# Optimization experiments

Hardware: AMD Instinct MI355X
Metric: run time of the kernel (lower is better)

Reference implementation:

```python
import jax, jax.numpy as jnp
import numpy as np

B, T = 16, 2048
NEG = -1e9  # finite large-negative for masked softmax (avoids NaN on empty rows)


def setup_inputs() -> dict:
    key = jax.random.key(0)
    k1, k2 = jax.random.split(key)
    logits = jax.random.normal(k1, (B, T, 1), dtype=jnp.float32)
    seq_len = jax.random.randint(k2, (B,), 1, T + 1, dtype=jnp.int32)
    return {"logits": logits, "seq_len": seq_len}


def reference(logits, seq_len):
    scores = jax.nn.sigmoid(logits.squeeze(-1))  # [B, T]
    # pairwise relevance: sigmoid((1 - |s_i - s_j| - 0.5) / 0.1)
    pairwise_diff = scores[:, :, None] - scores[:, None, :]  # [B, T, T]
    rel_mat = jax.nn.sigmoid((1.0 - jnp.abs(pairwise_diff) - 0.5) / 0.1)
    # ragged mask: valid positions are < seq_len[b]
    valid = jnp.arange(T)[None, :] < seq_len[:, None]            # [B, T]
    mask2d = valid[:, :, None] & valid[:, None, :]               # [B, T, T]
    masked = jnp.where(mask2d, rel_mat, NEG)
    sm = jax.nn.softmax(masked, axis=-1)                          # masked cols -> ~0
    # zero out invalid rows (original leaves them as zeros)
    out_mat = jnp.where(valid[:, :, None], sm, 0.0)
    return out_mat
```

## Files before the change

### kernel.cpp

```cpp
#include <hip/hip_runtime.h>

#define TT 2048
#define BLOCK 256
#define WAVES (BLOCK / 64)

#define LOG2E 1.4426950408889634f

typedef float vf4 __attribute__((ext_vector_type(4)));

__device__ __forceinline__ void nt_store4(float4* p, float x, float y, float z, float w) {
    vf4 v = {x, y, z, w};
    __builtin_nontemporal_store(v, (vf4*)p);
}

__device__ __forceinline__ float fast_sigmoid_e2(float u) {
    return __builtin_amdgcn_rcpf(1.0f + __builtin_amdgcn_exp2f(u));
}

__global__ __launch_bounds__(BLOCK) void score_branch_kernel(
    const float* __restrict__ logits, const int* __restrict__ seq_len,
    float* __restrict__ out)
{
    __shared__ float s_scores[TT];

    const int b    = blockIdx.y;
    const int row0 = blockIdx.x * WAVES;
    const int tid  = threadIdx.x;
    const int lane = tid & 63;
    const int wv   = tid >> 6;
    const int L    = seq_len[b];

    const int i = row0 + wv;
    float4* orow4 = (float4*)(out + ((size_t)b * TT + (size_t)i) * TT);

    if (row0 >= L) {
        #pragma unroll
        for (int q = 0; q < 8; ++q)
            nt_store4(&orow4[q * 64 + lane], 0.f, 0.f, 0.f, 0.f);
        return;
    }

    const float4* lg4 = (const float4*)(logits + (size_t)b * TT);
    float4* s4 = (float4*)s_scores;
    #pragma unroll
    for (int k = 0; k < TT / (BLOCK * 4); ++k) {
        int idx4 = tid + k * BLOCK;
        if (idx4 * 4 < L) {
            float4 v = lg4[idx4];
            float4 s;
            s.x = fast_sigmoid_e2(-LOG2E * v.x);
            s.y = fast_sigmoid_e2(-LOG2E * v.y);
            s.z = fast_sigmoid_e2(-LOG2E * v.z);
            s.w = fast_sigmoid_e2(-LOG2E * v.w);
            s4[idx4] = s;
        }
    }
    __syncthreads();

    if (i >= L) {
        #pragma unroll
        for (int q = 0; q < 8; ++q)
            nt_store4(&orow4[q * 64 + lane], 0.f, 0.f, 0.f, 0.f);
        return;
    }

    #pragma unroll
    for (int q = 0; q < 8; ++q) {
        if (q * 256 >= L)
            nt_store4(&orow4[q * 64 + lane], 0.f, 0.f, 0.f, 0.f);
    }

    const float si = s_scores[i];

    float4 e4[8];
    float partial = 0.f;
    #pragma unroll
    for (int q = 0; q < 8; ++q) {
        if (q * 256 < L) {
            const int idx4 = q * 64 + lane;
            float4 sj = s4[idx4];
            const int j0 = idx4 * 4;
            const bool fullgrp = ((q + 1) * 256 <= L);
            float vals[4] = {sj.x, sj.y, sj.z, sj.w};
            float* ev = (float*)&e4[q];
            #pragma unroll
            for (int qq = 0; qq < 4; ++qq) {
                float d  = si - vals[qq];
                float u  = fmaf(fabsf(d), 10.0f * LOG2E, -5.0f * LOG2E);
                float p  = fast_sigmoid_e2(u);
                float ee = __builtin_amdgcn_exp2f(p * LOG2E);
                if (!fullgrp)
                    ee = (j0 + qq < L) ? ee : 0.0f;
                ev[qq] = ee;
                partial += ee;
            }
        }
    }

    #pragma unroll
    for (int off = 32; off > 0; off >>= 1)
        partial += __shfl_xor(partial, off, 64);
    const float inv = __builtin_amdgcn_rcpf(partial);

    #pragma unroll
    for (int q = 0; q < 8; ++q) {
        if (q * 256 < L) {
            nt_store4(&orow4[q * 64 + lane],
                      e4[q].x * inv, e4[q].y * inv, e4[q].z * inv, e4[q].w * inv);
        }
    }
}

extern "C" void kernel_launch(void* const* d_in, const int* in_sizes, int n_in,
                              void* d_out, int out_size, void* d_ws, size_t ws_size,
                              hipStream_t stream) {
    const float* logits  = (const float*)d_in[0];
    const int*   seq_len = (const int*)d_in[1];
    float*       out     = (float*)d_out;

    const int B = in_sizes[1];
    dim3 grid(TT / WAVES, B);
    score_branch_kernel<<<grid, dim3(BLOCK), 0, stream>>>(logits, seq_len, out);
}
```

Before: 265.7 us.

## Split into prep (row sums) and emit kernels; use regular stores

Splits the fused softmax kernel into two launches. A prep kernel computes the sigmoid scores and each row's reciprocal softmax sum into workspace, and an emit kernel recomputes the exponentials and writes the normalized output directly, so no per-row register array is kept. Nontemporal stores are also replaced with plain float4 stores. The split doubles the transcendental work and adds a launch, in exchange for lower register pressure and a simpler store stream.

```diff
diff --git a/kernel.cpp b/kernel.cpp
--- a/kernel.cpp
+++ b/kernel.cpp
@@ -2,26 +2,20 @@
 
 #define TT 2048
 #define BLOCK 256
-#define WAVES (BLOCK / 64)
+#define WAVES 4
 
 #define LOG2E 1.4426950408889634f
 
-typedef float vf4 __attribute__((ext_vector_type(4)));
-
-__device__ __forceinline__ void nt_store4(float4* p, float x, float y, float z, float w) {
-    vf4 v = {x, y, z, w};
-    __builtin_nontemporal_store(v, (vf4*)p);
-}
-
-__device__ __forceinline__ float fast_sigmoid_e2(float u) {
+__device__ __forceinline__ float sig_e2(float u) {
     return __builtin_amdgcn_rcpf(1.0f + __builtin_amdgcn_exp2f(u));
 }
 
-__global__ __launch_bounds__(BLOCK) void score_branch_kernel(
+__global__ __launch_bounds__(BLOCK) void prep_kernel(
     const float* __restrict__ logits, const int* __restrict__ seq_len,
-    float* __restrict__ out)
+    float* __restrict__ ws_scores,
+    float* __restrict__ ws_inv)
 {
-    __shared__ float s_scores[TT];
+    __shared__ float s_sc[TT];
 
     const int b    = blockIdx.y;
     const int row0 = blockIdx.x * WAVES;
@@ -30,48 +24,169 @@
     const int wv   = tid >> 6;
     const int L    = seq_len[b];
 
+    const float4* lg4 = (const float4*)(logits + (size_t)b * TT);
+    float4* s4 = (float4*)s_sc;
+    #pragma unroll
+    for (int k = 0; k < 2; ++k) {
+        int idx4 = tid + k * BLOCK;
+        float4 v = lg4[idx4];
+        float4 s;
+        s.x = sig_e2(-LOG2E * v.x);
+        s.y = sig_e2(-LOG2E * v.y);
+        s.z = sig_e2(-LOG2E * v.z);
+        s.w = sig_e2(-LOG2E * v.w);
+        s4[idx4] = s;
+        if (blockIdx.x == 0)
+            ((float4*)(ws_scores + (size_t)b * TT))[idx4] = s;
+    }
+    __syncthreads();
+
+    const int i = row0 + wv;
+    if (i >= L) return;
+
+    const float si = s_sc[i];
+    float partial = 0.f;
+    #pragma unroll
+    for (int q = 0; q < 8; ++q) {
+        if (q * 256 < L) {
+            const int idx4 = q * 64 + lane;
+            float4 sj = s4[idx4];
+            const int j0 = idx4 * 4;
+            const bool fullgrp = ((q + 1) * 256 <= L);
+            float vals[4] = {sj.x, sj.y, sj.z, sj.w};
+            #pragma unroll
+            for (int qq = 0; qq < 4; ++qq) {
+                float d  = si - vals[qq];
+                float u  = fmaf(fabsf(d), 10.0f * LOG2E, -5.0f * LOG2E);
+                float p  = sig_e2(u);
+                float ee = __builtin_amdgcn_exp2f(p * LOG2E);
+                if (!fullgrp)
+                    ee = (j0 + qq < L) ? ee : 0.0f;
+                partial += ee;
+            }
+        }
+    }
+    #pragma unroll
+    for (int off = 32; off > 0; off >>= 1)
+        partial += __shfl_xor(partial, off, 64);
+    if (lane == 0)
+        ws_inv[(size_t)b * TT + i] = __builtin_amdgcn_rcpf(partial);
+}
+
+__global__ __launch_bounds__(BLOCK) void emit_kernel(
+    const int* __restrict__ seq_len,
+    const float* __restrict__ ws_scores, const float* __restrict__ ws_inv,
+    float* __restrict__ out)
+{
+    __shared__ float s_sc[TT];
+
+    const int b    = blockIdx.y;
+    const int row0 = blockIdx.x * WAVES;
+    const int tid  = threadIdx.x;
+    const int lane = tid & 63;
+    const int wv   = tid >> 6;
+    const int L    = seq_len[b];
+
     const int i = row0 + wv;
     float4* orow4 = (float4*)(out + ((size_t)b * TT + (size_t)i) * TT);
+    const float4 z4 = make_float4(0.f, 0.f, 0.f, 0.f);
 
     if (row0 >= L) {
         #pragma unroll
         for (int q = 0; q < 8; ++q)
-            nt_store4(&orow4[q * 64 + lane], 0.f, 0.f, 0.f, 0.f);
-        return;
-    }
-
+            orow4[q * 64 + lane] = z4;
+        return;
+    }
+
+    const float4* sc4 = (const float4*)(ws_scores + (size_t)b * TT);
+    float4* s4 = (float4*)s_sc;
+    #pragma unroll
+    for (int k = 0; k < 2; ++k) {
+        int idx4 = tid + k * BLOCK;
+        s4[idx4] = sc4[idx4];
+    }
+    __syncthreads();
+
+    if (i >= L) {
+        #pragma unroll
+        for (int q = 0; q < 8; ++q)
+            orow4[q * 64 + lane] = z4;
+        return;
+    }
+
+    #pragma unroll
+    for (int q = 0; q < 8; ++q)
+        if (q * 256 >= L)
+            orow4[q * 64 + lane] = z4;
+
+    const float si  = s_sc[i];
+    const float inv = ws_inv[(size_t)b * TT + i];
+
+    #pragma unroll
+    for (int q = 0; q < 8; ++q) {
+        if (q * 256 < L) {
+            const int idx4 = q * 64 + lane;
+            float4 sj = s4[idx4];
+            const int j0 = idx4 * 4;
+            const bool fullgrp = ((q + 1) * 256 <= L);
+            float vals[4] = {sj.x, sj.y, sj.z, sj.w};
+            float4 o;
+            float* ov = (float*)&o;
+            #pragma unroll
+            for (int qq = 0; qq < 4; ++qq) {
+                float d  = si - vals[qq];
+                float u  = fmaf(fabsf(d), 10.0f * LOG2E, -5.0f * LOG2E);
+                float p  = sig_e2(u);
+                float ee = __builtin_amdgcn_exp2f(p * LOG2E);
+                if (!fullgrp)
+                    ee = (j0 + qq < L) ? ee : 0.0f;
+                ov[qq] = ee * inv;
+            }
+            orow4[idx4] = o;
+        }
+    }
+}
+
+__global__ __launch_bounds__(BLOCK) void score_branch_kernel(
+    const float* __restrict__ logits, const int* __restrict__ seq_len,
+    float* __restrict__ out)
+{
+    __shared__ float s_scores[TT];
+    const int b    = blockIdx.y;
+    const int row0 = blockIdx.x * WAVES;
+    const int tid  = threadIdx.x;
+    const int lane = tid & 63;
+    const int wv   = tid >> 6;
+    const int L    = seq_len[b];
+    const int i = row0 + wv;
+    float4* orow4 = (float4*)(out + ((size_t)b * TT + (size_t)i) * TT);
+    const float4 z4 = make_float4(0.f, 0.f, 0.f, 0.f);
+
+    if (row0 >= L) {
+        #pragma unroll
+        for (int q = 0; q < 8; ++q) orow4[q * 64 + lane] = z4;
+        return;
+    }
     const float4* lg4 = (const float4*)(logits + (size_t)b * TT);
     float4* s4 = (float4*)s_scores;
     #pragma unroll
-    for (int k = 0; k < TT / (BLOCK * 4); ++k) {
+    for (int k = 0; k < 2; ++k) {
         int idx4 = tid + k * BLOCK;
-        if (idx4 * 4 < L) {
-            float4 v = lg4[idx4];
-            float4 s;
-            s.x = fast_sigmoid_e2(-LOG2E * v.x);
-            s.y = fast_sigmoid_e2(-LOG2E * v.y);
-            s.z = fast_sigmoid_e2(-LOG2E * v.z);
-            s.w = fast_sigmoid_e2(-LOG2E * v.w);
-            s4[idx4] = s;
-        }
+        float4 v = lg4[idx4];
+        float4 s;
+        s.x = sig_e2(-LOG2E * v.x);
+        s.y = sig_e2(-LOG2E * v.y);
+        s.z = sig_e2(-LOG2E * v.z);
+        s.w = sig_e2(-LOG2E * v.w);
+        s4[idx4] = s;
     }
     __syncthreads();
-
     if (i >= L) {
         #pragma unroll
-        for (int q = 0; q < 8; ++q)
-            nt_store4(&orow4[q * 64 + lane], 0.f, 0.f, 0.f, 0.f);
-        return;
-    }
-
-    #pragma unroll
-    for (int q = 0; q < 8; ++q) {
-        if (q * 256 >= L)
-            nt_store4(&orow4[q * 64 + lane], 0.f, 0.f, 0.f, 0.f);
-    }
-
+        for (int q = 0; q < 8; ++q) orow4[q * 64 + lane] = z4;
+        return;
+    }
     const float si = s_scores[i];
-
     float4 e4[8];
     float partial = 0.f;
     #pragma unroll
@@ -87,26 +202,27 @@
             for (int qq = 0; qq < 4; ++qq) {
                 float d  = si - vals[qq];
                 float u  = fmaf(fabsf(d), 10.0f * LOG2E, -5.0f * LOG2E);
-                float p  = fast_sigmoid_e2(u);
+                float p  = sig_e2(u);
                 float ee = __builtin_amdgcn_exp2f(p * LOG2E);
-                if (!fullgrp)
-                    ee = (j0 + qq < L) ? ee : 0.0f;
+                if (!fullgrp) ee = (j0 + qq < L) ? ee : 0.0f;
                 ev[qq] = ee;
                 partial += ee;
             }
-        }
-    }
-
+        } else {
+            orow4[q * 64 + lane] = z4;
+        }
+    }
     #pragma unroll
     for (int off = 32; off > 0; off >>= 1)
         partial += __shfl_xor(partial, off, 64);
     const float inv = __builtin_amdgcn_rcpf(partial);
-
-    #pragma unroll
-    for (int q = 0; q < 8; ++q) {
-        if (q * 256 < L) {
-            nt_store4(&orow4[q * 64 + lane],
-                      e4[q].x * inv, e4[q].y * inv, e4[q].z * inv, e4[q].w * inv);
+    #pragma unroll
+    for (int q = 0; q < 8; ++q) {
+        if (q * 256 < L) {
+            float4 o;
+            o.x = e4[q].x * inv; o.y = e4[q].y * inv;
+            o.z = e4[q].z * inv; o.w = e4[q].w * inv;
+            orow4[q * 64 + lane] = o;
         }
     }
 }
@@ -119,6 +235,15 @@
     float*       out     = (float*)d_out;
 
     const int B = in_sizes[1];
-    dim3 grid(TT / WAVES, B);
-    score_branch_kernel<<<grid, dim3(BLOCK), 0, stream>>>(logits, seq_len, out);
-}
+    dim3 grid(TT / WAVES, B), blk(BLOCK);
+
+    const size_t need = (size_t)2 * B * TT * sizeof(float);
+    if (d_ws != nullptr && ws_size >= need) {
+        float* ws_scores = (float*)d_ws;
+        float* ws_inv    = ws_scores + (size_t)B * TT;
+        prep_kernel<<<grid, blk, 0, stream>>>(logits, seq_len, ws_scores, ws_inv);
+        emit_kernel<<<grid, blk, 0, stream>>>(seq_len, ws_scores, ws_inv, out);
+    } else {
+        score_branch_kernel<<<grid, blk, 0, stream>>>(logits, seq_len, out);
+    }
+}
```

Measured after the change: 272.9 us. 1.03x slower.

## Process eight rows per wave to amortize score staging; use regular stores

Applied to the files above, without the earlier changes.

Each wave now handles eight consecutive rows, so a block covers 32 rows and the grid shrinks eightfold. Each block's sigmoid staging of the scores into shared memory is therefore reused across more rows. The staging loop also drops its length guard and sigmoids all 2048 logits. Nontemporal stores are replaced with ordinary float4 stores, which changes cache behaviour on a write-bound 256MB output and may cost something. Fewer blocks also means less parallelism and worse load balance across ragged rows.

```diff
diff --git a/kernel.cpp b/kernel.cpp
--- a/kernel.cpp
+++ b/kernel.cpp
@@ -2,18 +2,13 @@
 
 #define TT 2048
 #define BLOCK 256
-#define WAVES (BLOCK / 64)
+#define WAVES 4
+#define RPW 8
+#define ROWS_PER_BLOCK (WAVES * RPW)
 
 #define LOG2E 1.4426950408889634f
 
-typedef float vf4 __attribute__((ext_vector_type(4)));
-
-__device__ __forceinline__ void nt_store4(float4* p, float x, float y, float z, float w) {
-    vf4 v = {x, y, z, w};
-    __builtin_nontemporal_store(v, (vf4*)p);
-}
-
-__device__ __forceinline__ float fast_sigmoid_e2(float u) {
+__device__ __forceinline__ float sig_e2(float u) {
     return __builtin_amdgcn_rcpf(1.0f + __builtin_amdgcn_exp2f(u));
 }
 
@@ -21,92 +16,97 @@
     const float* __restrict__ logits, const int* __restrict__ seq_len,
     float* __restrict__ out)
 {
-    __shared__ float s_scores[TT];
+    __shared__ float s_sc[TT];
 
     const int b    = blockIdx.y;
-    const int row0 = blockIdx.x * WAVES;
+    const int row0 = blockIdx.x * ROWS_PER_BLOCK;
     const int tid  = threadIdx.x;
     const int lane = tid & 63;
     const int wv   = tid >> 6;
     const int L    = seq_len[b];
 
-    const int i = row0 + wv;
-    float4* orow4 = (float4*)(out + ((size_t)b * TT + (size_t)i) * TT);
+    const int wrow0 = row0 + wv * RPW;
+    const float4 z4 = make_float4(0.f, 0.f, 0.f, 0.f);
 
     if (row0 >= L) {
-        #pragma unroll
-        for (int q = 0; q < 8; ++q)
-            nt_store4(&orow4[q * 64 + lane], 0.f, 0.f, 0.f, 0.f);
+        float4* o4 = (float4*)(out + ((size_t)b * TT + wrow0) * TT);
+        for (int r = 0; r < RPW; ++r) {
+            #pragma unroll
+            for (int q = 0; q < 8; ++q)
+                o4[r * (TT / 4) + q * 64 + lane] = z4;
+        }
         return;
     }
 
     const float4* lg4 = (const float4*)(logits + (size_t)b * TT);
-    float4* s4 = (float4*)s_scores;
+    float4* s4 = (float4*)s_sc;
     #pragma unroll
-    for (int k = 0; k < TT / (BLOCK * 4); ++k) {
+    for (int k = 0; k < 2; ++k) {
         int idx4 = tid + k * BLOCK;
-        if (idx4 * 4 < L) {
-            float4 v = lg4[idx4];
-            float4 s;
-            s.x = fast_sigmoid_e2(-LOG2E * v.x);
-            s.y = fast_sigmoid_e2(-LOG2E * v.y);
-            s.z = fast_sigmoid_e2(-LOG2E * v.z);
-            s.w = fast_sigmoid_e2(-LOG2E * v.w);
-            s4[idx4] = s;
-        }
+        float4 v = lg4[idx4];
+        float4 s;
+        s.x = sig_e2(-LOG2E * v.x);
+        s.y = sig_e2(-LOG2E * v.y);
+        s.z = sig_e2(-LOG2E * v.z);
+        s.w = sig_e2(-LOG2E * v.w);
+        s4[idx4] = s;
     }
     __syncthreads();
 
-    if (i >= L) {
+    for (int r = 0; r < RPW; ++r) {
+        const int i = wrow0 + r;
+        float4* orow4 = (float4*)(out + ((size_t)b * TT + (size_t)i) * TT);
+
+        if (i >= L) {
+            #pragma unroll
+            for (int q = 0; q < 8; ++q)
+                orow4[q * 64 + lane] = z4;
+            continue;
+        }
+
+        const float si = s_sc[i];
+        float4 e4[8];
+        float partial = 0.f;
         #pragma unroll
-        for (int q = 0; q < 8; ++q)
-            nt_store4(&orow4[q * 64 + lane], 0.f, 0.f, 0.f, 0.f);
-        return;
-    }
-
-    #pragma unroll
-    for (int q = 0; q < 8; ++q) {
-        if (q * 256 >= L)
-            nt_store4(&orow4[q * 64 + lane], 0.f, 0.f, 0.f, 0.f);
-    }
-
-    const float si = s_scores[i];
-
-    float4 e4[8];
-    float partial = 0.f;
-    #pragma unroll
-    for (int q = 0; q < 8; ++q) {
-        if (q * 256 < L) {
-            const int idx4 = q * 64 + lane;
-            float4 sj = s4[idx4];
-            const int j0 = idx4 * 4;
-            const bool fullgrp = ((q + 1) * 256 <= L);
-            float vals[4] = {sj.x, sj.y, sj.z, sj.w};
-            float* ev = (float*)&e4[q];
-            #pragma unroll
-            for (int qq = 0; qq < 4; ++qq) {
-                float d  = si - vals[qq];
-                float u  = fmaf(fabsf(d), 10.0f * LOG2E, -5.0f * LOG2E);
-                float p  = fast_sigmoid_e2(u);
-                float ee = __builtin_amdgcn_exp2f(p * LOG2E);
-                if (!fullgrp)
-                    ee = (j0 + qq < L) ? ee : 0.0f;
-                ev[qq] = ee;
-                partial += ee;
+        for (int q = 0; q < 8; ++q) {
+            if (q * 256 < L) {
+                const int idx4 = q * 64 + lane;
+                float4 sj = s4[idx4];
+                const int j0 = idx4 * 4;
+                const bool fullgrp = ((q + 1) * 256 <= L);
+                float vals[4] = {sj.x, sj.y, sj.z, sj.w};
+                float* ev = (float*)&e4[q];
+                #pragma unroll
+                for (int qq = 0; qq < 4; ++qq) {
+                    float d  = si - vals[qq];
+                    float u  = fmaf(fabsf(d), 10.0f * LOG2E, -5.0f * LOG2E);
+                    float p  = sig_e2(u);
+                    float ee = __builtin_amdgcn_exp2f(p * LOG2E);
+                    if (!fullgrp)
+                        ee = (j0 + qq < L) ? ee : 0.0f;
+                    ev[qq] = ee;
+                    partial += ee;
+                }
+            } else {
+                orow4[q * 64 + lane] = z4;
             }
         }
-    }
 
-    #pragma unroll
-    for (int off = 32; off > 0; off >>= 1)
-        partial += __shfl_xor(partial, off, 64);
-    const float inv = __builtin_amdgcn_rcpf(partial);
+        #pragma unroll
+        for (int off = 32; off > 0; off >>= 1)
+            partial += __shfl_xor(partial, off, 64);
+        const float inv = __builtin_amdgcn_rcpf(partial);
 
-    #pragma unroll
-    for (int q = 0; q < 8; ++q) {
-        if (q * 256 < L) {
-            nt_store4(&orow4[q * 64 + lane],
-                      e4[q].x * inv, e4[q].y * inv, e4[q].z * inv, e4[q].w * inv);
+        #pragma unroll
+        for (int q = 0; q < 8; ++q) {
+            if (q * 256 < L) {
+                float4 o;
+                o.x = e4[q].x * inv;
+                o.y = e4[q].y * inv;
+                o.z = e4[q].z * inv;
+                o.w = e4[q].w * inv;
+                orow4[q * 64 + lane] = o;
+            }
         }
     }
 }
@@ -119,6 +119,6 @@
     float*       out     = (float*)d_out;
 
     const int B = in_sizes[1];
-    dim3 grid(TT / WAVES, B);
+    dim3 grid(TT / ROWS_PER_BLOCK, B);
     score_branch_kernel<<<grid, dim3(BLOCK), 0, stream>>>(logits, seq_len, out);
 }
```

Result: faster. 256.7 us (-3.4%).
